# Performance work log

Measured on AMD Instinct MI355X. Metric: run time of the kernel, lower is better.

Reference implementation:

```python
import jax, jax.numpy as jnp
import numpy as np

# config: nsql-350M-like, 8 layers
L, D, H, HD, FF, V, RD, MP = 8, 1024, 16, 64, 4096, 51200, 32, 4


def setup_inputs() -> dict:
    key = jax.random.key(0)
    ks = jax.random.split(key, 8)
    B, S = 1, 1024
    s = 0.02
    return {
        'idx': jax.random.randint(ks[0], (B, S), 0, V),
        'input_pos': jnp.arange(S),
        'emb': jax.random.normal(ks[1], (V, D)) * s,
        'Wqkv': jax.random.normal(ks[2], (L, 3 * D, D)) * s,
        'Wo': jax.random.normal(ks[3], (L, D, D)) * s,
        'ln1_w': jnp.ones((L, D)), 'ln1_b': jnp.zeros((L, D)),
        'fc_in_w': jax.random.normal(ks[4], (L, FF, D)) * s,
        'fc_in_b': jnp.zeros((L, FF)),
        'fc_out_w': jax.random.normal(ks[5], (L, D, FF)) * s,
        'fc_out_b': jnp.zeros((L, D)),
        'lnf_w': jnp.ones((D,)), 'lnf_b': jnp.zeros((D,)),
        'lm_w': jax.random.normal(ks[6], (V, D)) * s,
        'lm_b': jnp.zeros((V,)),
    }


def _layer_norm(x, w, b, eps=1e-5):
    mu = jnp.mean(x, axis=-1, keepdims=True)
    var = jnp.var(x, axis=-1, keepdims=True)
    return (x - mu) * jax.lax.rsqrt(var + eps) * w + b


def _new_gelu(x):
    # transformers NewGELUActivation == tanh-approx gelu
    return jax.nn.gelu(x, approximate=True)


def _sincos(input_pos):
    # create_sinusoidal_positions over rotary_dim, gathered at input_pos
    inv_freq = 1.0 / (10000.0 ** (jnp.arange(0, RD, 2, dtype=jnp.float32) / RD))
    ang = input_pos.astype(jnp.float32)[:, None] * inv_freq          # [S, RD/2]
    # repeat_interleave(..., 2, dim=-1) -> interleaved sin/cos, shape [1,S,1,RD]
    sin = jnp.repeat(jnp.sin(ang), 2, axis=-1)[None, :, None, :]
    cos = jnp.repeat(jnp.cos(ang), 2, axis=-1)[None, :, None, :]
    return sin, cos


def _rotary(x, sin, cos):
    # x: [B,S,H,HD]; GPT-J interleaved rotary on first RD dims
    xr, xp = x[..., :RD], x[..., RD:]
    x1, x2 = xr[..., ::2], xr[..., 1::2]
    rot = jnp.stack((-x2, x1), axis=-1).reshape(xr.shape)  # rotate_every_two
    return jnp.concatenate([xr * cos + rot * sin, xp], axis=-1)


def reference(idx, input_pos, emb, Wqkv, Wo, ln1_w, ln1_b, fc_in_w, fc_in_b,
              fc_out_w, fc_out_b, lnf_w, lnf_b, lm_w, lm_b):
    B, S = idx.shape
    x = emb[idx]                                        # [B,S,D]
    sin, cos = _sincos(input_pos)
    causal = jnp.tril(jnp.ones((S, S), dtype=bool))
    neg = jnp.finfo(x.dtype).min
    ld = D // MP

    def split_heads(t):
        # CodeGen _split_heads with mp_num=4: [B,S,MP,ld] -> [B,S,H,HD]
        return t.reshape(B, S, MP, H // MP, HD).reshape(B, S, H, HD)

    for l in range(L):
        h = _layer_norm(x, ln1_w[l], ln1_b[l])
        qkv = (h @ Wqkv[l].T).reshape(B, S, MP, 3 * ld)
        q, v, k = qkv[..., :ld], qkv[..., ld:2 * ld], qkv[..., 2 * ld:]  # q,v,k order!
        q = _rotary(split_heads(q), sin, cos)
        k = _rotary(split_heads(k), sin, cos)
        vh = split_heads(v)
        q, k, vh = (jnp.transpose(t, (0, 2, 1, 3)) for t in (q, k, vh))  # [B,H,S,HD]
        scores = jnp.einsum('bhqd,bhkd->bhqk', q, k) / jnp.sqrt(jnp.asarray(HD, x.dtype))
        scores = jnp.where(causal, scores, neg)
        att = jax.nn.softmax(scores, axis=-1)
        y = jnp.einsum('bhqk,bhkd->bhqd', att, vh)
        y = jnp.transpose(y, (0, 2, 1, 3)).reshape(B, S, D)
        attn_out = y @ Wo[l].T
        mlp = _new_gelu(h @ fc_in_w[l].T + fc_in_b[l]) @ fc_out_w[l].T + fc_out_b[l]
        x = attn_out + mlp + x                          # parallel block + residual

    x = _layer_norm(x, lnf_w, lnf_b)
    return x @ lm_w.T + lm_b                            # [B,S,V]
```

## Files before the change

### kernel.cpp

```cpp
#include <hip/hip_runtime.h>

#define SQ 1024
#define DIM 1024
#define NH 16
#define HDIM 64
#define FFD 4096
#define NV 51200
#define NL 8
#define LDBUF 5120

typedef __bf16 bf16x8 __attribute__((ext_vector_type(8)));
typedef float f32x4 __attribute__((ext_vector_type(4)));

__device__ __forceinline__ unsigned short f2bf(float f) {
    union { float f; unsigned int i; } v; v.f = f;
    unsigned int r = v.i + 0x7fffu + ((v.i >> 16) & 1u);
    return (unsigned short)(r >> 16);
}
__device__ __forceinline__ float gelu_tanh(float x) {
    float x3 = x * x * x;
    return 0.5f * x * (1.0f + tanhf(0.79788456080286535588f * (x + 0.044715f * x3)));
}

#define GLD16(gp, lp) __builtin_amdgcn_global_load_lds( \
    (__attribute__((address_space(1))) void*)(gp), \
    (__attribute__((address_space(3))) void*)(lp), 16, 0, 0)
#define VMCNT0 asm volatile("s_waitcnt vmcnt(0)" ::: "memory")

__global__ void cvt4_kernel(const float* __restrict__ w0, const float* __restrict__ w1,
                            const float* __restrict__ w2, const float* __restrict__ w3,
                            unsigned short* __restrict__ d0, unsigned short* __restrict__ d1,
                            unsigned short* __restrict__ d2, unsigned short* __restrict__ d3) {
    const int b = blockIdx.x;
    const float* s; unsigned short* d; long off;
    if (b < 1536)      { s = w0; d = d0; off = (long)b * 2048; }
    else if (b < 2048) { s = w1; d = d1; off = (long)(b - 1536) * 2048; }
    else if (b < 4096) { s = w2; d = d2; off = (long)(b - 2048) * 2048; }
    else               { s = w3; d = d3; off = (long)(b - 4096) * 2048; }
    const long i = off + threadIdx.x * 8;
    float4 a = *reinterpret_cast<const float4*>(s + i);
    float4 c = *reinterpret_cast<const float4*>(s + i + 4);
    bf16x8 w;
    w[0] = (__bf16)a.x; w[1] = (__bf16)a.y; w[2] = (__bf16)a.z; w[3] = (__bf16)a.w;
    w[4] = (__bf16)c.x; w[5] = (__bf16)c.y; w[6] = (__bf16)c.z; w[7] = (__bf16)c.w;
    *reinterpret_cast<bf16x8*>(d + i) = w;
}
__global__ void cvt_kernel(const float* __restrict__ src, unsigned short* __restrict__ dst) {
    const long i = ((long)blockIdx.x * 256 + threadIdx.x) * 8;
    float4 a = *reinterpret_cast<const float4*>(src + i);
    float4 b = *reinterpret_cast<const float4*>(src + i + 4);
    bf16x8 w;
    w[0] = (__bf16)a.x; w[1] = (__bf16)a.y; w[2] = (__bf16)a.z; w[3] = (__bf16)a.w;
    w[4] = (__bf16)b.x; w[5] = (__bf16)b.y; w[6] = (__bf16)b.z; w[7] = (__bf16)b.w;
    *reinterpret_cast<bf16x8*>(dst + i) = w;
}

__global__ void sincos_kernel(const int* __restrict__ pos, float2* __restrict__ sc) {
    const int t = blockIdx.x * 256 + threadIdx.x;
    if (t >= SQ * 16) return;
    const int s = t >> 4, i = t & 15;
    const float ang = (float)pos[s] * powf(10000.0f, -(float)i / 16.0f);
    sc[t] = make_float2(sinf(ang), cosf(ang));
}

__global__ void embed_kernel(const int* __restrict__ idx, const float* __restrict__ emb,
                             float* __restrict__ x) {
    const int s = blockIdx.x;
    const int d = threadIdx.x * 4;
    const int row = idx[s];
    *reinterpret_cast<float4*>(x + (long)s * DIM + d) =
        *reinterpret_cast<const float4*>(emb + (long)row * DIM + d);
}

template <bool RED>
__global__ __launch_bounds__(256) void ln_kernel(float* __restrict__ x,
                                                 const float* __restrict__ part,
                                                 const float* __restrict__ w,
                                                 const float* __restrict__ b,
                                                 unsigned short* __restrict__ out) {
    __shared__ float red[8];
    const int s = blockIdx.x, tid = threadIdx.x;
    const long fidx = (long)s * 256 + tid;
    float4 v = reinterpret_cast<const float4*>(x)[fidx];
    if (RED) {
        #pragma unroll
        for (int z = 0; z < 8; z++) {
            float4 p = reinterpret_cast<const float4*>(part + (long)z * SQ * DIM)[fidx];
            v.x += p.x; v.y += p.y; v.z += p.z; v.w += p.w;
        }
        reinterpret_cast<float4*>(x)[fidx] = v;
    }
    float sum = v.x + v.y + v.z + v.w;
    float sq = v.x * v.x + v.y * v.y + v.z * v.z + v.w * v.w;
    #pragma unroll
    for (int off = 32; off; off >>= 1) { sum += __shfl_xor(sum, off); sq += __shfl_xor(sq, off); }
    const int wid = tid >> 6, lane = tid & 63;
    if (lane == 0) { red[wid * 2] = sum; red[wid * 2 + 1] = sq; }
    __syncthreads();
    sum = red[0] + red[2] + red[4] + red[6];
    sq  = red[1] + red[3] + red[5] + red[7];
    const float mu = sum * (1.0f / DIM);
    const float var = sq * (1.0f / DIM) - mu * mu;
    const float rstd = rsqrtf(var + 1e-5f);
    const int d = tid * 4;
    float vv[4] = {v.x, v.y, v.z, v.w};
    ushort4 o;
    unsigned short* op = (unsigned short*)&o;
    #pragma unroll
    for (int j = 0; j < 4; j++)
        op[j] = f2bf((vv[j] - mu) * rstd * w[d + j] + b[d + j]);
    *reinterpret_cast<ushort4*>(out + (long)s * DIM + d) = o;
}

template <int MODE>
__global__ __launch_bounds__(256) void gemm128(const unsigned short* __restrict__ A, int lda,
                                               const unsigned short* __restrict__ B1,
                                               const unsigned short* __restrict__ B2,
                                               const float* __restrict__ bias,
                                               void* __restrict__ C1, void* __restrict__ C2,
                                               const float2* __restrict__ sc,
                                               unsigned short* __restrict__ qt,
                                               unsigned short* __restrict__ kt,
                                               unsigned short* __restrict__ vt) {
    __shared__ __align__(16) unsigned short As[2][128 * 64];
    __shared__ __align__(16) unsigned short Bs[2][128 * 64];
    const int tid = threadIdx.x;
    const int nwg = gridDim.x, qch = nwg >> 3;
    const int sb = (blockIdx.x & 7) * qch + (blockIdx.x >> 3);
    int mb, nb, kz, kt0, ktn;
    if (MODE == 1) { kz = sb & 7; nb = (sb >> 3) & 7; mb = sb >> 6; kt0 = kz * 10; ktn = kt0 + 10; }
    else           { kz = 0; mb = sb & 7; nb = sb >> 3; kt0 = 0; ktn = 16; }
    const int m0 = mb * 128, n0 = nb * 128;
    const int lane = tid & 63, wid = tid >> 6;
    const int l15 = lane & 15, lhi = lane >> 4;
    const int wr = wid >> 1, wc = wid & 1;
    const int sw = l15 & 7;

    const unsigned short* Bbase = B1;
    int nloc = n0;
    if (MODE == 0 && nb >= 24) { Bbase = B2; nloc = n0 - 3072; }

    f32x4 acc[4][4];
    #pragma unroll
    for (int i = 0; i < 4; i++)
        #pragma unroll
        for (int j = 0; j < 4; j++) acc[i][j] = (f32x4){0.f, 0.f, 0.f, 0.f};

    const int wbase = (tid & ~63) * 8;

    auto stage = [&](int buf, int kt_) {
        const int k0 = kt_ << 6;
        #pragma unroll
        for (int i = 0; i < 4; i++) {
            const int e = (i * 256 + tid) * 8;
            const int r = e >> 6;
            const int cs = (((e >> 3) & 7) ^ (r & 7)) * 8;
            GLD16(A + (long)(m0 + r) * lda + k0 + cs, &As[buf][i * 2048 + wbase]);
        }
        if (MODE == 1) {
            const unsigned short* Bp = (k0 < 1024) ? B1 : B2;
            const int ldb = (k0 < 1024) ? 1024 : 4096;
            const int kk = (k0 < 1024) ? k0 : k0 - 1024;
            #pragma unroll
            for (int i = 0; i < 4; i++) {
                const int e = (i * 256 + tid) * 8;
                const int r = e >> 6;
                const int cs = (((e >> 3) & 7) ^ (r & 7)) * 8;
                GLD16(Bp + (long)(n0 + r) * ldb + kk + cs, &Bs[buf][i * 2048 + wbase]);
            }
        } else {
            #pragma unroll
            for (int i = 0; i < 4; i++) {
                const int e = (i * 256 + tid) * 8;
                const int r = e >> 6;
                const int cs = (((e >> 3) & 7) ^ (r & 7)) * 8;
                GLD16(Bbase + (long)(nloc + r) * 1024 + k0 + cs, &Bs[buf][i * 2048 + wbase]);
            }
        }
    };
    auto compute = [&](int buf) {
        #pragma unroll
        for (int ks = 0; ks < 2; ks++) {
            bf16x8 af[4], bfr[4];
            #pragma unroll
            for (int mf = 0; mf < 4; mf++)
                af[mf] = *reinterpret_cast<const bf16x8*>(
                    &As[buf][(wr * 64 + mf * 16 + l15) * 64 + ((ks * 4 + lhi) ^ sw) * 8]);
            #pragma unroll
            for (int nf = 0; nf < 4; nf++)
                bfr[nf] = *reinterpret_cast<const bf16x8*>(
                    &Bs[buf][(wc * 64 + nf * 16 + l15) * 64 + ((ks * 4 + lhi) ^ sw) * 8]);
            #pragma unroll
            for (int mf = 0; mf < 4; mf++)
                #pragma unroll
                for (int nf = 0; nf < 4; nf++)
                    acc[mf][nf] = __builtin_amdgcn_mfma_f32_16x16x32_bf16(af[mf], bfr[nf], acc[mf][nf], 0, 0, 0);
        }
    };

    int cur = 0;
    stage(0, kt0);
    VMCNT0; __syncthreads();
    for (int kt_ = kt0; kt_ < ktn; kt_++) {
        if (kt_ + 1 < ktn) stage(cur ^ 1, kt_ + 1);
        compute(cur);
        if (kt_ + 1 < ktn) { VMCNT0; __syncthreads(); cur ^= 1; }
    }

    if (MODE == 0 && nb < 24) {
        #pragma unroll
        for (int nf = 0; nf < 4; nf++) {
            const int col = n0 + wc * 64 + nf * 16 + l15;
            const int g = col / 768;
            const int r768 = col - g * 768;
            const int sec = r768 >> 8;
            const int off = r768 & 255;
            const int h = g * 4 + (off >> 6);
            const int d = off & 63;
            const bool isrot = (d < 32);
            const int dodd = d & 1;
            #pragma unroll
            for (int mf = 0; mf < 4; mf++) {
                #pragma unroll
                for (int j = 0; j < 4; j++) {
                    const int row = m0 + wr * 64 + mf * 16 + lhi * 4 + j;
                    float v = acc[mf][nf][j];
                    const float pv = __shfl_xor(v, 1);
                    float outv = v;
                    if (isrot && sec != 1) {
                        const float2 scv = sc[row * 16 + (d >> 1)];
                        outv = dodd ? (v * scv.y + pv * scv.x)
                                    : (v * scv.y - pv * scv.x);
                    }
                    if (sec == 0)      qt[((long)(h * SQ + row)) * HDIM + d] = f2bf(outv);
                    else if (sec == 2) kt[((long)(h * SQ + row)) * HDIM + d] = f2bf(outv);
                    else               vt[(long)h * (HDIM * SQ) + (long)d * SQ + row] = f2bf(outv);
                }
            }
        }
    } else {
        #pragma unroll
        for (int nf = 0; nf < 4; nf++) {
            const int col = n0 + wc * 64 + nf * 16 + l15;
            #pragma unroll
            for (int mf = 0; mf < 4; mf++) {
                #pragma unroll
                for (int j = 0; j < 4; j++) {
                    float v = acc[mf][nf][j];
                    const int row = m0 + wr * 64 + mf * 16 + lhi * 4 + j;
                    if (MODE == 0) {
                        v = gelu_tanh(v + bias[col - 3072]);
                        ((unsigned short*)C2)[(long)row * LDBUF + (col - 3072)] = f2bf(v);
                    } else {
                        if (kz == 0) v += bias[col];
                        ((float*)C1)[(long)kz * SQ * DIM + (long)row * DIM + col] = v;
                    }
                }
            }
        }
    }
}

__global__ __launch_bounds__(512) void gemm256(const unsigned short* __restrict__ A,
                                               const unsigned short* __restrict__ B,
                                               const float* __restrict__ bias,
                                               float* __restrict__ C) {
    __shared__ __align__(16) unsigned short As[2][256 * 64];
    __shared__ __align__(16) unsigned short Bs[2][256 * 64];
    const int tid = threadIdx.x;
    const int nwg = gridDim.x, qch = nwg >> 3;
    const int sb = (blockIdx.x & 7) * qch + (blockIdx.x >> 3);
    const int mb = sb & 3, nb = sb >> 2;
    const int m0 = mb * 256, n0 = nb * 256;
    const int lane = tid & 63, wid = tid >> 6;
    const int l15 = lane & 15, lhi = lane >> 4;
    const int wm = wid >> 2, wn = wid & 3;
    const int sw = l15 & 7;

    f32x4 acc[8][4];
    #pragma unroll
    for (int i = 0; i < 8; i++)
        #pragma unroll
        for (int j = 0; j < 4; j++) acc[i][j] = (f32x4){0.f, 0.f, 0.f, 0.f};

    const int wbase = (tid & ~63) * 8;

    auto stage = [&](int buf, int kt) {
        const int k0 = kt << 6;
        #pragma unroll
        for (int i = 0; i < 4; i++) {
            const int e = (i * 512 + tid) * 8;
            const int r = e >> 6;
            const int cs = (((e >> 3) & 7) ^ (r & 7)) * 8;
            GLD16(A + (long)(m0 + r) * 1024 + k0 + cs, &As[buf][i * 4096 + wbase]);
            GLD16(B + (long)(n0 + r) * 1024 + k0 + cs, &Bs[buf][i * 4096 + wbase]);
        }
    };
    auto compute = [&](int buf) {
        #pragma unroll
        for (int ks = 0; ks < 2; ks++) {
            bf16x8 af[8], bfr[4];
            #pragma unroll
            for (int mf = 0; mf < 8; mf++)
                af[mf] = *reinterpret_cast<const bf16x8*>(
                    &As[buf][(wm * 128 + mf * 16 + l15) * 64 + ((ks * 4 + lhi) ^ sw) * 8]);
            #pragma unroll
            for (int nf = 0; nf < 4; nf++)
                bfr[nf] = *reinterpret_cast<const bf16x8*>(
                    &Bs[buf][(wn * 64 + nf * 16 + l15) * 64 + ((ks * 4 + lhi) ^ sw) * 8]);
            #pragma unroll
            for (int mf = 0; mf < 8; mf++)
                #pragma unroll
                for (int nf = 0; nf < 4; nf++)
                    acc[mf][nf] = __builtin_amdgcn_mfma_f32_16x16x32_bf16(af[mf], bfr[nf], acc[mf][nf], 0, 0, 0);
        }
    };

    int cur = 0;
    stage(0, 0);
    VMCNT0; __syncthreads();
    for (int kt = 0; kt < 16; kt++) {
        if (kt < 15) stage(cur ^ 1, kt + 1);
        compute(cur);
        if (kt < 15) { VMCNT0; __syncthreads(); cur ^= 1; }
    }

    #pragma unroll
    for (int nf = 0; nf < 4; nf++) {
        const int col = n0 + wn * 64 + nf * 16 + l15;
        const float bv = bias[col];
        #pragma unroll
        for (int mf = 0; mf < 8; mf++) {
            #pragma unroll
            for (int j = 0; j < 4; j++) {
                const int row = m0 + wm * 128 + mf * 16 + lhi * 4 + j;
                C[(long)row * NV + col] = acc[mf][nf][j] + bv;
            }
        }
    }
}

__global__ __launch_bounds__(256) void attn_kernel(const unsigned short* __restrict__ qt,
                                                   const unsigned short* __restrict__ kt,
                                                   const unsigned short* __restrict__ vt,
                                                   unsigned short* __restrict__ y) {
    __shared__ __align__(16) unsigned short Ks[2][64 * 64];
    __shared__ __align__(16) unsigned short Vs[2][64 * 64];
    __shared__ __align__(16) unsigned short Ps[4][16 * 64];
    const int h = blockIdx.y;
    const int qb = (int)gridDim.x - 1 - (int)blockIdx.x;
    const int tid = threadIdx.x, lane = tid & 63, wid = tid >> 6;
    const int l15 = lane & 15, lhi = lane >> 4;
    const int q0 = qb * 64 + wid * 16;
    const int sw = l15 & 7;

    bf16x8 aq[2];
    {
        const unsigned short* qp = qt + ((long)(h * SQ + q0 + l15)) * HDIM;
        aq[0] = *reinterpret_cast<const bf16x8*>(qp + lhi * 8);
        aq[1] = *reinterpret_cast<const bf16x8*>(qp + 32 + lhi * 8);
    }
    f32x4 o[4];
    #pragma unroll
    for (int nf = 0; nf < 4; nf++) o[nf] = (f32x4){0.f, 0.f, 0.f, 0.f};
    float mrow[4] = {-1e30f, -1e30f, -1e30f, -1e30f};
    float lrow[4] = {0.f, 0.f, 0.f, 0.f};

    const int wb8 = (tid & ~63) * 8;
    auto stageKV = [&](int buf, int kv0) {
        #pragma unroll
        for (int i = 0; i < 2; i++) {
            const int e = (i * 256 + tid) * 8;
            const int r = e >> 6;
            const int cs = (((e >> 3) & 7) ^ (r & 7)) * 8;
            GLD16(kt + ((long)(h * SQ + kv0 + r)) * HDIM + cs, &Ks[buf][i * 2048 + wb8]);
            GLD16(vt + (long)h * (HDIM * SQ) + (long)r * SQ + kv0 + cs, &Vs[buf][i * 2048 + wb8]);
        }
    };

    int cur = 0;
    stageKV(0, 0);
    VMCNT0; __syncthreads();
    for (int kvt = 0; kvt <= qb; kvt++) {
        const int kv0 = kvt * 64;
        if (kvt < qb) stageKV(cur ^ 1, kv0 + 64);

        f32x4 sa[4];
        #pragma unroll
        for (int hc = 0; hc < 4; hc++) sa[hc] = (f32x4){0.f, 0.f, 0.f, 0.f};
        #pragma unroll
        for (int hc = 0; hc < 4; hc++)
            #pragma unroll
            for (int ks = 0; ks < 2; ks++) {
                bf16x8 bk = *reinterpret_cast<const bf16x8*>(
                    &Ks[cur][(hc * 16 + l15) * 64 + ((ks * 4 + lhi) ^ sw) * 8]);
                sa[hc] = __builtin_amdgcn_mfma_f32_16x16x32_bf16(aq[ks], bk, sa[hc], 0, 0, 0);
            }
        float pr[4][4], mb[4];
        #pragma unroll
        for (int j = 0; j < 4; j++) {
            const int qi = q0 + lhi * 4 + j;
            #pragma unroll
            for (int hc = 0; hc < 4; hc++) {
                const int ki = kv0 + hc * 16 + l15;
                const float sv = sa[hc][j] * 0.125f;
                pr[hc][j] = (ki <= qi) ? sv : -1e30f;
            }
            mb[j] = fmaxf(fmaxf(pr[0][j], pr[1][j]), fmaxf(pr[2][j], pr[3][j]));
        }
        #pragma unroll
        for (int off = 1; off < 16; off <<= 1)
            #pragma unroll
            for (int j = 0; j < 4; j++) mb[j] = fmaxf(mb[j], __shfl_xor(mb[j], off));
        float alpha[4], psum[4];
        #pragma unroll
        for (int j = 0; j < 4; j++) {
            const float mn = fmaxf(mrow[j], mb[j]);
            alpha[j] = __expf(mrow[j] - mn);
            mrow[j] = mn;
            psum[j] = 0.f;
            #pragma unroll
            for (int hc = 0; hc < 4; hc++) { pr[hc][j] = __expf(pr[hc][j] - mn); psum[j] += pr[hc][j]; }
        }
        #pragma unroll
        for (int off = 1; off < 16; off <<= 1)
            #pragma unroll
            for (int j = 0; j < 4; j++) psum[j] += __shfl_xor(psum[j], off);
        #pragma unroll
        for (int j = 0; j < 4; j++) lrow[j] = lrow[j] * alpha[j] + psum[j];
        #pragma unroll
        for (int nf = 0; nf < 4; nf++)
            #pragma unroll
            for (int j = 0; j < 4; j++) o[nf][j] *= alpha[j];
        #pragma unroll
        for (int hc = 0; hc < 4; hc++)
            #pragma unroll
            for (int j = 0; j < 4; j++) {
                const int prow = lhi * 4 + j;
                const int pc8 = (hc * 2 + (l15 >> 3)) ^ (prow & 7);
                Ps[wid][prow * 64 + pc8 * 8 + (l15 & 7)] = f2bf(pr[hc][j]);
            }
        bf16x8 ap[2];
        ap[0] = *reinterpret_cast<const bf16x8*>(&Ps[wid][l15 * 64 + ((0 + lhi) ^ sw) * 8]);
        ap[1] = *reinterpret_cast<const bf16x8*>(&Ps[wid][l15 * 64 + ((4 + lhi) ^ sw) * 8]);
        #pragma unroll
        for (int nf = 0; nf < 4; nf++)
            #pragma unroll
            for (int ks2 = 0; ks2 < 2; ks2++) {
                bf16x8 bv = *reinterpret_cast<const bf16x8*>(
                    &Vs[cur][(nf * 16 + l15) * 64 + ((ks2 * 4 + lhi) ^ sw) * 8]);
                o[nf] = __builtin_amdgcn_mfma_f32_16x16x32_bf16(ap[ks2], bv, o[nf], 0, 0, 0);
            }
        if (kvt < qb) { VMCNT0; __syncthreads(); cur ^= 1; }
    }
    #pragma unroll
    for (int nf = 0; nf < 4; nf++)
        #pragma unroll
        for (int j = 0; j < 4; j++) {
            const int row = q0 + lhi * 4 + j;
            y[(long)row * LDBUF + h * HDIM + nf * 16 + l15] = f2bf(o[nf][j] / lrow[j]);
        }
}

extern "C" void kernel_launch(void* const* d_in, const int* in_sizes, int n_in,
                              void* d_out, int out_size, void* d_ws, size_t ws_size,
                              hipStream_t stream) {
    const int* idx    = (const int*)d_in[0];
    const int* pos    = (const int*)d_in[1];
    const float* emb  = (const float*)d_in[2];
    const float* Wqkv = (const float*)d_in[3];
    const float* Wo   = (const float*)d_in[4];
    const float* ln1w = (const float*)d_in[5];
    const float* ln1b = (const float*)d_in[6];
    const float* fciw = (const float*)d_in[7];
    const float* fcib = (const float*)d_in[8];
    const float* fcow = (const float*)d_in[9];
    const float* fcob = (const float*)d_in[10];
    const float* lnfw = (const float*)d_in[11];
    const float* lnfb = (const float*)d_in[12];
    const float* lmw  = (const float*)d_in[13];
    const float* lmb  = (const float*)d_in[14];

    char* ws = (char*)d_ws;
    unsigned short* wbuf = (unsigned short*)ws;   ws += (long)NV * DIM * 2;
    unsigned short* wqkvb = wbuf;
    unsigned short* wob   = wbuf + (long)3072 * 1024;
    unsigned short* fcinb = wob + (long)1024 * 1024;
    unsigned short* fcoutb= fcinb + (long)4096 * 1024;
    float* x           = (float*)ws;          ws += (long)SQ * DIM * 4;
    float* parts       = (float*)ws;          ws += (long)8 * SQ * DIM * 4;
    unsigned short* h  = (unsigned short*)ws; ws += (long)SQ * DIM * 2;
    unsigned short* qt = (unsigned short*)ws; ws += (long)NH * SQ * HDIM * 2;
    unsigned short* kt = (unsigned short*)ws; ws += (long)NH * SQ * HDIM * 2;
    unsigned short* vt = (unsigned short*)ws; ws += (long)NH * SQ * HDIM * 2;
    unsigned short* buf= (unsigned short*)ws; ws += (long)SQ * LDBUF * 2;
    float2* sc         = (float2*)ws;         ws += (long)SQ * 16 * 8;

    sincos_kernel<<<64, 256, 0, stream>>>(pos, sc);
    embed_kernel<<<SQ, 256, 0, stream>>>(idx, emb, x);

    for (int l = 0; l < NL; l++) {
        cvt4_kernel<<<6144, 256, 0, stream>>>(Wqkv + (long)l * 3 * DIM * DIM,
                                              Wo   + (long)l * DIM * DIM,
                                              fciw + (long)l * FFD * DIM,
                                              fcow + (long)l * DIM * FFD,
                                              wqkvb, wob, fcinb, fcoutb);

        if (l == 0) ln_kernel<false><<<SQ, 256, 0, stream>>>(x, nullptr, ln1w, ln1b, h);
        else ln_kernel<true><<<SQ, 256, 0, stream>>>(x, parts, ln1w + (long)l * DIM, ln1b + (long)l * DIM, h);

        gemm128<0><<<448, 256, 0, stream>>>(h, DIM, wqkvb, fcinb, fcib + (long)l * FFD,
                                            nullptr, buf + DIM, sc, qt, kt, vt);
        attn_kernel<<<dim3(16, NH), 256, 0, stream>>>(qt, kt, vt, buf);
        gemm128<1><<<512, 256, 0, stream>>>(buf, LDBUF, wob, fcoutb, fcob + (long)l * DIM,
                                            parts, nullptr, nullptr, nullptr, nullptr, nullptr);
    }
    cvt_kernel<<<25600, 256, 0, stream>>>(lmw, wbuf);
    ln_kernel<true><<<SQ, 256, 0, stream>>>(x, parts, lnfw, lnfb, h);
    gemm256<<<800, 512, 0, stream>>>(h, wbuf, lmb, (float*)d_out);
}
```

Before: 1.197 ms.

## Run attention concurrently with fc_out GEMM and add Wo via read-modify-write

Attention and the fc_out split-K GEMM now run in one launch: the first 256 blocks do causal flash attention while the other 512 compute fc_out partials, which do not depend on attention. The Wo projection then runs as a separate 4-way split-K GEMM that adds its result into the existing partial buffers with read-modify-write. The aim is to fill idle compute units during the unevenly loaded causal attention and to shrink the serial critical path. In exchange, the Wo stage adds an extra fp32 read per element of four partial slices, and the heterogeneous blocks share a larger LDS footprint, which may lower occupancy.

```diff
diff --git a/kernel.cpp b/kernel.cpp
--- a/kernel.cpp
+++ b/kernel.cpp
@@ -112,24 +112,21 @@
     *reinterpret_cast<ushort4*>(out + (long)s * DIM + d) = o;
 }
 
-template <int MODE>
-__global__ __launch_bounds__(256) void gemm128(const unsigned short* __restrict__ A, int lda,
-                                               const unsigned short* __restrict__ B1,
-                                               const unsigned short* __restrict__ B2,
-                                               const float* __restrict__ bias,
-                                               void* __restrict__ C1, void* __restrict__ C2,
-                                               const float2* __restrict__ sc,
-                                               unsigned short* __restrict__ qt,
-                                               unsigned short* __restrict__ kt,
-                                               unsigned short* __restrict__ vt) {
+__global__ __launch_bounds__(256) void gemm_qkv_fcin(const unsigned short* __restrict__ A,
+                                                     const unsigned short* __restrict__ B1,
+                                                     const unsigned short* __restrict__ B2,
+                                                     const float* __restrict__ bias,
+                                                     unsigned short* __restrict__ ffout,
+                                                     const float2* __restrict__ sc,
+                                                     unsigned short* __restrict__ qt,
+                                                     unsigned short* __restrict__ kt,
+                                                     unsigned short* __restrict__ vt) {
     __shared__ __align__(16) unsigned short As[2][128 * 64];
     __shared__ __align__(16) unsigned short Bs[2][128 * 64];
     const int tid = threadIdx.x;
     const int nwg = gridDim.x, qch = nwg >> 3;
     const int sb = (blockIdx.x & 7) * qch + (blockIdx.x >> 3);
-    int mb, nb, kz, kt0, ktn;
-    if (MODE == 1) { kz = sb & 7; nb = (sb >> 3) & 7; mb = sb >> 6; kt0 = kz * 10; ktn = kt0 + 10; }
-    else           { kz = 0; mb = sb & 7; nb = sb >> 3; kt0 = 0; ktn = 16; }
+    const int mb = sb & 7, nb = sb >> 3;
     const int m0 = mb * 128, n0 = nb * 128;
     const int lane = tid & 63, wid = tid >> 6;
     const int l15 = lane & 15, lhi = lane >> 4;
@@ -138,7 +135,7 @@
 
     const unsigned short* Bbase = B1;
     int nloc = n0;
-    if (MODE == 0 && nb >= 24) { Bbase = B2; nloc = n0 - 3072; }
+    if (nb >= 24) { Bbase = B2; nloc = n0 - 3072; }
 
     f32x4 acc[4][4];
     #pragma unroll
@@ -155,27 +152,14 @@
             const int e = (i * 256 + tid) * 8;
             const int r = e >> 6;
             const int cs = (((e >> 3) & 7) ^ (r & 7)) * 8;
-            GLD16(A + (long)(m0 + r) * lda + k0 + cs, &As[buf][i * 2048 + wbase]);
-        }
-        if (MODE == 1) {
-            const unsigned short* Bp = (k0 < 1024) ? B1 : B2;
-            const int ldb = (k0 < 1024) ? 1024 : 4096;
-            const int kk = (k0 < 1024) ? k0 : k0 - 1024;
-            #pragma unroll
-            for (int i = 0; i < 4; i++) {
-                const int e = (i * 256 + tid) * 8;
-                const int r = e >> 6;
-                const int cs = (((e >> 3) & 7) ^ (r & 7)) * 8;
-                GLD16(Bp + (long)(n0 + r) * ldb + kk + cs, &Bs[buf][i * 2048 + wbase]);
-            }
-        } else {
-            #pragma unroll
-            for (int i = 0; i < 4; i++) {
-                const int e = (i * 256 + tid) * 8;
-                const int r = e >> 6;
-                const int cs = (((e >> 3) & 7) ^ (r & 7)) * 8;
-                GLD16(Bbase + (long)(nloc + r) * 1024 + k0 + cs, &Bs[buf][i * 2048 + wbase]);
-            }
+            GLD16(A + (long)(m0 + r) * DIM + k0 + cs, &As[buf][i * 2048 + wbase]);
+        }
+        #pragma unroll
+        for (int i = 0; i < 4; i++) {
+            const int e = (i * 256 + tid) * 8;
+            const int r = e >> 6;
+            const int cs = (((e >> 3) & 7) ^ (r & 7)) * 8;
+            GLD16(Bbase + (long)(nloc + r) * 1024 + k0 + cs, &Bs[buf][i * 2048 + wbase]);
         }
     };
     auto compute = [&](int buf) {
@@ -199,15 +183,15 @@
     };
 
     int cur = 0;
-    stage(0, kt0);
+    stage(0, 0);
     VMCNT0; __syncthreads();
-    for (int kt_ = kt0; kt_ < ktn; kt_++) {
-        if (kt_ + 1 < ktn) stage(cur ^ 1, kt_ + 1);
+    for (int kt_ = 0; kt_ < 16; kt_++) {
+        if (kt_ + 1 < 16) stage(cur ^ 1, kt_ + 1);
         compute(cur);
-        if (kt_ + 1 < ktn) { VMCNT0; __syncthreads(); cur ^= 1; }
-    }
-
-    if (MODE == 0 && nb < 24) {
+        if (kt_ + 1 < 16) { VMCNT0; __syncthreads(); cur ^= 1; }
+    }
+
+    if (nb < 24) {
         #pragma unroll
         for (int nf = 0; nf < 4; nf++) {
             const int col = n0 + wc * 64 + nf * 16 + l15;
@@ -246,16 +230,288 @@
             for (int mf = 0; mf < 4; mf++) {
                 #pragma unroll
                 for (int j = 0; j < 4; j++) {
-                    float v = acc[mf][nf][j];
                     const int row = m0 + wr * 64 + mf * 16 + lhi * 4 + j;
-                    if (MODE == 0) {
-                        v = gelu_tanh(v + bias[col - 3072]);
-                        ((unsigned short*)C2)[(long)row * LDBUF + (col - 3072)] = f2bf(v);
-                    } else {
-                        if (kz == 0) v += bias[col];
-                        ((float*)C1)[(long)kz * SQ * DIM + (long)row * DIM + col] = v;
-                    }
+                    float v = gelu_tanh(acc[mf][nf][j] + bias[col - 3072]);
+                    ffout[(long)row * LDBUF + (col - 3072)] = f2bf(v);
                 }
+            }
+        }
+    }
+}
+
+__global__ __launch_bounds__(256) void attn_fcout(const unsigned short* __restrict__ qt,
+                                                  const unsigned short* __restrict__ kt,
+                                                  const unsigned short* __restrict__ vt,
+                                                  unsigned short* __restrict__ buf,
+                                                  const unsigned short* __restrict__ fcw,
+                                                  const float* __restrict__ fcb,
+                                                  float* __restrict__ parts) {
+    __shared__ __align__(16) unsigned short smem[32768];
+    const int tid = threadIdx.x, lane = tid & 63, wid = tid >> 6;
+    const int l15 = lane & 15, lhi = lane >> 4;
+    const int sw = l15 & 7;
+    const int wbase = (tid & ~63) * 8;
+
+    if (blockIdx.x < 256) {
+        unsigned short* Ks0 = smem;
+        unsigned short* Vs0 = smem + 8192;
+        unsigned short* Psw = smem + 16384 + wid * 1024;
+        const int h = blockIdx.x & 15;
+        const int qb = 15 - ((int)blockIdx.x >> 4);
+        const int q0 = qb * 64 + wid * 16;
+
+        bf16x8 aq[2];
+        {
+            const unsigned short* qp = qt + ((long)(h * SQ + q0 + l15)) * HDIM;
+            aq[0] = *reinterpret_cast<const bf16x8*>(qp + lhi * 8);
+            aq[1] = *reinterpret_cast<const bf16x8*>(qp + 32 + lhi * 8);
+        }
+        f32x4 o[4];
+        #pragma unroll
+        for (int nf = 0; nf < 4; nf++) o[nf] = (f32x4){0.f, 0.f, 0.f, 0.f};
+        float mrow[4] = {-1e30f, -1e30f, -1e30f, -1e30f};
+        float lrow[4] = {0.f, 0.f, 0.f, 0.f};
+
+        auto stageKV = [&](int b, int kv0) {
+            #pragma unroll
+            for (int i = 0; i < 2; i++) {
+                const int e = (i * 256 + tid) * 8;
+                const int r = e >> 6;
+                const int cs = (((e >> 3) & 7) ^ (r & 7)) * 8;
+                GLD16(kt + ((long)(h * SQ + kv0 + r)) * HDIM + cs, Ks0 + b * 4096 + i * 2048 + wbase);
+                GLD16(vt + (long)h * (HDIM * SQ) + (long)r * SQ + kv0 + cs, Vs0 + b * 4096 + i * 2048 + wbase);
+            }
+        };
+
+        int cur = 0;
+        stageKV(0, 0);
+        VMCNT0; __syncthreads();
+        for (int kvt = 0; kvt <= qb; kvt++) {
+            const int kv0 = kvt * 64;
+            if (kvt < qb) stageKV(cur ^ 1, kv0 + 64);
+
+            f32x4 sa[4];
+            #pragma unroll
+            for (int hc = 0; hc < 4; hc++) sa[hc] = (f32x4){0.f, 0.f, 0.f, 0.f};
+            #pragma unroll
+            for (int hc = 0; hc < 4; hc++)
+                #pragma unroll
+                for (int ks = 0; ks < 2; ks++) {
+                    bf16x8 bk = *reinterpret_cast<const bf16x8*>(
+                        Ks0 + cur * 4096 + (hc * 16 + l15) * 64 + ((ks * 4 + lhi) ^ sw) * 8);
+                    sa[hc] = __builtin_amdgcn_mfma_f32_16x16x32_bf16(aq[ks], bk, sa[hc], 0, 0, 0);
+                }
+            float pr[4][4], mb[4];
+            #pragma unroll
+            for (int j = 0; j < 4; j++) {
+                const int qi = q0 + lhi * 4 + j;
+                #pragma unroll
+                for (int hc = 0; hc < 4; hc++) {
+                    const int ki = kv0 + hc * 16 + l15;
+                    const float sv = sa[hc][j] * 0.125f;
+                    pr[hc][j] = (ki <= qi) ? sv : -1e30f;
+                }
+                mb[j] = fmaxf(fmaxf(pr[0][j], pr[1][j]), fmaxf(pr[2][j], pr[3][j]));
+            }
+            #pragma unroll
+            for (int off = 1; off < 16; off <<= 1)
+                #pragma unroll
+                for (int j = 0; j < 4; j++) mb[j] = fmaxf(mb[j], __shfl_xor(mb[j], off));
+            float alpha[4], psum[4];
+            #pragma unroll
+            for (int j = 0; j < 4; j++) {
+                const float mn = fmaxf(mrow[j], mb[j]);
+                alpha[j] = __expf(mrow[j] - mn);
+                mrow[j] = mn;
+                psum[j] = 0.f;
+                #pragma unroll
+                for (int hc = 0; hc < 4; hc++) { pr[hc][j] = __expf(pr[hc][j] - mn); psum[j] += pr[hc][j]; }
+            }
+            #pragma unroll
+            for (int off = 1; off < 16; off <<= 1)
+                #pragma unroll
+                for (int j = 0; j < 4; j++) psum[j] += __shfl_xor(psum[j], off);
+            #pragma unroll
+            for (int j = 0; j < 4; j++) lrow[j] = lrow[j] * alpha[j] + psum[j];
+            #pragma unroll
+            for (int nf = 0; nf < 4; nf++)
+                #pragma unroll
+                for (int j = 0; j < 4; j++) o[nf][j] *= alpha[j];
+            #pragma unroll
+            for (int hc = 0; hc < 4; hc++)
+                #pragma unroll
+                for (int j = 0; j < 4; j++) {
+                    const int prow = lhi * 4 + j;
+                    const int pc8 = (hc * 2 + (l15 >> 3)) ^ (prow & 7);
+                    Psw[prow * 64 + pc8 * 8 + (l15 & 7)] = f2bf(pr[hc][j]);
+                }
+            bf16x8 ap[2];
+            ap[0] = *reinterpret_cast<const bf16x8*>(Psw + l15 * 64 + ((0 + lhi) ^ sw) * 8);
+            ap[1] = *reinterpret_cast<const bf16x8*>(Psw + l15 * 64 + ((4 + lhi) ^ sw) * 8);
+            #pragma unroll
+            for (int nf = 0; nf < 4; nf++)
+                #pragma unroll
+                for (int ks2 = 0; ks2 < 2; ks2++) {
+                    bf16x8 bv = *reinterpret_cast<const bf16x8*>(
+                        Vs0 + cur * 4096 + (nf * 16 + l15) * 64 + ((ks2 * 4 + lhi) ^ sw) * 8);
+                    o[nf] = __builtin_amdgcn_mfma_f32_16x16x32_bf16(ap[ks2], bv, o[nf], 0, 0, 0);
+                }
+            if (kvt < qb) { VMCNT0; __syncthreads(); cur ^= 1; }
+        }
+        #pragma unroll
+        for (int nf = 0; nf < 4; nf++)
+            #pragma unroll
+            for (int j = 0; j < 4; j++) {
+                const int row = q0 + lhi * 4 + j;
+                buf[(long)row * LDBUF + h * HDIM + nf * 16 + l15] = f2bf(o[nf][j] / lrow[j]);
+            }
+    } else {
+        unsigned short* As0 = smem;
+        unsigned short* Bs0 = smem + 16384;
+        const int b2 = (int)blockIdx.x - 256;
+        const int sb = (b2 & 7) * 64 + (b2 >> 3);
+        const int kz = sb & 7, nb = (sb >> 3) & 7, mb = sb >> 6;
+        const int m0 = mb * 128, n0 = nb * 128;
+        const int kt0 = kz * 8;
+        const int wr = wid >> 1, wc = wid & 1;
+        const unsigned short* Aff = buf + DIM;
+
+        f32x4 acc[4][4];
+        #pragma unroll
+        for (int i = 0; i < 4; i++)
+            #pragma unroll
+            for (int j = 0; j < 4; j++) acc[i][j] = (f32x4){0.f, 0.f, 0.f, 0.f};
+
+        auto stage = [&](int bf_, int kt_) {
+            const int k0 = kt_ << 6;
+            #pragma unroll
+            for (int i = 0; i < 4; i++) {
+                const int e = (i * 256 + tid) * 8;
+                const int r = e >> 6;
+                const int cs = (((e >> 3) & 7) ^ (r & 7)) * 8;
+                GLD16(Aff + (long)(m0 + r) * LDBUF + k0 + cs, As0 + bf_ * 8192 + i * 2048 + wbase);
+                GLD16(fcw + (long)(n0 + r) * FFD + k0 + cs, Bs0 + bf_ * 8192 + i * 2048 + wbase);
+            }
+        };
+        auto compute = [&](int bf_) {
+            #pragma unroll
+            for (int ks = 0; ks < 2; ks++) {
+                bf16x8 af[4], bfr[4];
+                #pragma unroll
+                for (int mf = 0; mf < 4; mf++)
+                    af[mf] = *reinterpret_cast<const bf16x8*>(
+                        As0 + bf_ * 8192 + (wr * 64 + mf * 16 + l15) * 64 + ((ks * 4 + lhi) ^ sw) * 8);
+                #pragma unroll
+                for (int nf = 0; nf < 4; nf++)
+                    bfr[nf] = *reinterpret_cast<const bf16x8*>(
+                        Bs0 + bf_ * 8192 + (wc * 64 + nf * 16 + l15) * 64 + ((ks * 4 + lhi) ^ sw) * 8);
+                #pragma unroll
+                for (int mf = 0; mf < 4; mf++)
+                    #pragma unroll
+                    for (int nf = 0; nf < 4; nf++)
+                        acc[mf][nf] = __builtin_amdgcn_mfma_f32_16x16x32_bf16(af[mf], bfr[nf], acc[mf][nf], 0, 0, 0);
+            }
+        };
+
+        int cur = 0;
+        stage(0, kt0);
+        VMCNT0; __syncthreads();
+        for (int t = 0; t < 8; t++) {
+            if (t + 1 < 8) stage(cur ^ 1, kt0 + t + 1);
+            compute(cur);
+            if (t + 1 < 8) { VMCNT0; __syncthreads(); cur ^= 1; }
+        }
+
+        float* P = parts + (long)kz * SQ * DIM;
+        #pragma unroll
+        for (int nf = 0; nf < 4; nf++) {
+            const int col = n0 + wc * 64 + nf * 16 + l15;
+            const float bv = (kz == 0) ? fcb[col] : 0.f;
+            #pragma unroll
+            for (int mf = 0; mf < 4; mf++) {
+                #pragma unroll
+                for (int j = 0; j < 4; j++) {
+                    const int row = m0 + wr * 64 + mf * 16 + lhi * 4 + j;
+                    P[(long)row * DIM + col] = acc[mf][nf][j] + bv;
+                }
+            }
+        }
+    }
+}
+
+__global__ __launch_bounds__(256) void wo_rmw(const unsigned short* __restrict__ buf,
+                                              const unsigned short* __restrict__ wo,
+                                              float* __restrict__ parts) {
+    __shared__ __align__(16) unsigned short As[2][128 * 64];
+    __shared__ __align__(16) unsigned short Bs[2][128 * 64];
+    const int tid = threadIdx.x;
+    const int sb = (blockIdx.x & 7) * 32 + (blockIdx.x >> 3);
+    const int kz = sb & 3, nb = (sb >> 2) & 7, mb = sb >> 5;
+    const int m0 = mb * 128, n0 = nb * 128;
+    const int kt0 = kz * 4;
+    const int lane = tid & 63, wid = tid >> 6;
+    const int l15 = lane & 15, lhi = lane >> 4;
+    const int wr = wid >> 1, wc = wid & 1;
+    const int sw = l15 & 7;
+    const int wbase = (tid & ~63) * 8;
+
+    f32x4 acc[4][4];
+    #pragma unroll
+    for (int i = 0; i < 4; i++)
+        #pragma unroll
+        for (int j = 0; j < 4; j++) acc[i][j] = (f32x4){0.f, 0.f, 0.f, 0.f};
+
+    auto stage = [&](int bf_, int kt_) {
+        const int k0 = kt_ << 6;
+        #pragma unroll
+        for (int i = 0; i < 4; i++) {
+            const int e = (i * 256 + tid) * 8;
+            const int r = e >> 6;
+            const int cs = (((e >> 3) & 7) ^ (r & 7)) * 8;
+            GLD16(buf + (long)(m0 + r) * LDBUF + k0 + cs, &As[bf_][i * 2048 + wbase]);
+            GLD16(wo + (long)(n0 + r) * DIM + k0 + cs, &Bs[bf_][i * 2048 + wbase]);
+        }
+    };
+    auto compute = [&](int bf_) {
+        #pragma unroll
+        for (int ks = 0; ks < 2; ks++) {
+            bf16x8 af[4], bfr[4];
+            #pragma unroll
+            for (int mf = 0; mf < 4; mf++)
+                af[mf] = *reinterpret_cast<const bf16x8*>(
+                    &As[bf_][(wr * 64 + mf * 16 + l15) * 64 + ((ks * 4 + lhi) ^ sw) * 8]);
+            #pragma unroll
+            for (int nf = 0; nf < 4; nf++)
+                bfr[nf] = *reinterpret_cast<const bf16x8*>(
+                    &Bs[bf_][(wc * 64 + nf * 16 + l15) * 64 + ((ks * 4 + lhi) ^ sw) * 8]);
+            #pragma unroll
+            for (int mf = 0; mf < 4; mf++)
+                #pragma unroll
+                for (int nf = 0; nf < 4; nf++)
+                    acc[mf][nf] = __builtin_amdgcn_mfma_f32_16x16x32_bf16(af[mf], bfr[nf], acc[mf][nf], 0, 0, 0);
+        }
+    };
+
+    int cur = 0;
+    stage(0, kt0);
+    VMCNT0; __syncthreads();
+    for (int t = 0; t < 4; t++) {
+        if (t + 1 < 4) stage(cur ^ 1, kt0 + t + 1);
+        compute(cur);
+        if (t + 1 < 4) { VMCNT0; __syncthreads(); cur ^= 1; }
+    }
+
+    float* P = parts + (long)kz * SQ * DIM;
+    #pragma unroll
+    for (int nf = 0; nf < 4; nf++) {
+        const int col = n0 + wc * 64 + nf * 16 + l15;
+        #pragma unroll
+        for (int mf = 0; mf < 4; mf++) {
+            #pragma unroll
+            for (int j = 0; j < 4; j++) {
+                const int row = m0 + wr * 64 + mf * 16 + lhi * 4 + j;
+                const long idx = (long)row * DIM + col;
+                P[idx] += acc[mf][nf][j];
             }
         }
     }
@@ -338,128 +594,6 @@
             }
         }
     }
-}
-
-__global__ __launch_bounds__(256) void attn_kernel(const unsigned short* __restrict__ qt,
-                                                   const unsigned short* __restrict__ kt,
-                                                   const unsigned short* __restrict__ vt,
-                                                   unsigned short* __restrict__ y) {
-    __shared__ __align__(16) unsigned short Ks[2][64 * 64];
-    __shared__ __align__(16) unsigned short Vs[2][64 * 64];
-    __shared__ __align__(16) unsigned short Ps[4][16 * 64];
-    const int h = blockIdx.y;
-    const int qb = (int)gridDim.x - 1 - (int)blockIdx.x;
-    const int tid = threadIdx.x, lane = tid & 63, wid = tid >> 6;
-    const int l15 = lane & 15, lhi = lane >> 4;
-    const int q0 = qb * 64 + wid * 16;
-    const int sw = l15 & 7;
-
-    bf16x8 aq[2];
-    {
-        const unsigned short* qp = qt + ((long)(h * SQ + q0 + l15)) * HDIM;
-        aq[0] = *reinterpret_cast<const bf16x8*>(qp + lhi * 8);
-        aq[1] = *reinterpret_cast<const bf16x8*>(qp + 32 + lhi * 8);
-    }
-    f32x4 o[4];
-    #pragma unroll
-    for (int nf = 0; nf < 4; nf++) o[nf] = (f32x4){0.f, 0.f, 0.f, 0.f};
-    float mrow[4] = {-1e30f, -1e30f, -1e30f, -1e30f};
-    float lrow[4] = {0.f, 0.f, 0.f, 0.f};
-
-    const int wb8 = (tid & ~63) * 8;
-    auto stageKV = [&](int buf, int kv0) {
-        #pragma unroll
-        for (int i = 0; i < 2; i++) {
-            const int e = (i * 256 + tid) * 8;
-            const int r = e >> 6;
-            const int cs = (((e >> 3) & 7) ^ (r & 7)) * 8;
-            GLD16(kt + ((long)(h * SQ + kv0 + r)) * HDIM + cs, &Ks[buf][i * 2048 + wb8]);
-            GLD16(vt + (long)h * (HDIM * SQ) + (long)r * SQ + kv0 + cs, &Vs[buf][i * 2048 + wb8]);
-        }
-    };
-
-    int cur = 0;
-    stageKV(0, 0);
-    VMCNT0; __syncthreads();
-    for (int kvt = 0; kvt <= qb; kvt++) {
-        const int kv0 = kvt * 64;
-        if (kvt < qb) stageKV(cur ^ 1, kv0 + 64);
-
-        f32x4 sa[4];
-        #pragma unroll
-        for (int hc = 0; hc < 4; hc++) sa[hc] = (f32x4){0.f, 0.f, 0.f, 0.f};
-        #pragma unroll
-        for (int hc = 0; hc < 4; hc++)
-            #pragma unroll
-            for (int ks = 0; ks < 2; ks++) {
-                bf16x8 bk = *reinterpret_cast<const bf16x8*>(
-                    &Ks[cur][(hc * 16 + l15) * 64 + ((ks * 4 + lhi) ^ sw) * 8]);
-                sa[hc] = __builtin_amdgcn_mfma_f32_16x16x32_bf16(aq[ks], bk, sa[hc], 0, 0, 0);
-            }
-        float pr[4][4], mb[4];
-        #pragma unroll
-        for (int j = 0; j < 4; j++) {
-            const int qi = q0 + lhi * 4 + j;
-            #pragma unroll
-            for (int hc = 0; hc < 4; hc++) {
-                const int ki = kv0 + hc * 16 + l15;
-                const float sv = sa[hc][j] * 0.125f;
-                pr[hc][j] = (ki <= qi) ? sv : -1e30f;
-            }
-            mb[j] = fmaxf(fmaxf(pr[0][j], pr[1][j]), fmaxf(pr[2][j], pr[3][j]));
-        }
-        #pragma unroll
-        for (int off = 1; off < 16; off <<= 1)
-            #pragma unroll
-            for (int j = 0; j < 4; j++) mb[j] = fmaxf(mb[j], __shfl_xor(mb[j], off));
-        float alpha[4], psum[4];
-        #pragma unroll
-        for (int j = 0; j < 4; j++) {
-            const float mn = fmaxf(mrow[j], mb[j]);
-            alpha[j] = __expf(mrow[j] - mn);
-            mrow[j] = mn;
-            psum[j] = 0.f;
-            #pragma unroll
-            for (int hc = 0; hc < 4; hc++) { pr[hc][j] = __expf(pr[hc][j] - mn); psum[j] += pr[hc][j]; }
-        }
-        #pragma unroll
-        for (int off = 1; off < 16; off <<= 1)
-            #pragma unroll
-            for (int j = 0; j < 4; j++) psum[j] += __shfl_xor(psum[j], off);
-        #pragma unroll
-        for (int j = 0; j < 4; j++) lrow[j] = lrow[j] * alpha[j] + psum[j];
-        #pragma unroll
-        for (int nf = 0; nf < 4; nf++)
-            #pragma unroll
-            for (int j = 0; j < 4; j++) o[nf][j] *= alpha[j];
-        #pragma unroll
-        for (int hc = 0; hc < 4; hc++)
-            #pragma unroll
-            for (int j = 0; j < 4; j++) {
-                const int prow = lhi * 4 + j;
-                const int pc8 = (hc * 2 + (l15 >> 3)) ^ (prow & 7);
-                Ps[wid][prow * 64 + pc8 * 8 + (l15 & 7)] = f2bf(pr[hc][j]);
-            }
-        bf16x8 ap[2];
-        ap[0] = *reinterpret_cast<const bf16x8*>(&Ps[wid][l15 * 64 + ((0 + lhi) ^ sw) * 8]);
-        ap[1] = *reinterpret_cast<const bf16x8*>(&Ps[wid][l15 * 64 + ((4 + lhi) ^ sw) * 8]);
-        #pragma unroll
-        for (int nf = 0; nf < 4; nf++)
-            #pragma unroll
-            for (int ks2 = 0; ks2 < 2; ks2++) {
-                bf16x8 bv = *reinterpret_cast<const bf16x8*>(
-                    &Vs[cur][(nf * 16 + l15) * 64 + ((ks2 * 4 + lhi) ^ sw) * 8]);
-                o[nf] = __builtin_amdgcn_mfma_f32_16x16x32_bf16(ap[ks2], bv, o[nf], 0, 0, 0);
-            }
-        if (kvt < qb) { VMCNT0; __syncthreads(); cur ^= 1; }
-    }
-    #pragma unroll
-    for (int nf = 0; nf < 4; nf++)
-        #pragma unroll
-        for (int j = 0; j < 4; j++) {
-            const int row = q0 + lhi * 4 + j;
-            y[(long)row * LDBUF + h * HDIM + nf * 16 + l15] = f2bf(o[nf][j] / lrow[j]);
-        }
 }
 
 extern "C" void kernel_launch(void* const* d_in, const int* in_sizes, int n_in,
@@ -509,11 +643,10 @@
         if (l == 0) ln_kernel<false><<<SQ, 256, 0, stream>>>(x, nullptr, ln1w, ln1b, h);
         else ln_kernel<true><<<SQ, 256, 0, stream>>>(x, parts, ln1w + (long)l * DIM, ln1b + (long)l * DIM, h);
 
-        gemm128<0><<<448, 256, 0, stream>>>(h, DIM, wqkvb, fcinb, fcib + (long)l * FFD,
-                                            nullptr, buf + DIM, sc, qt, kt, vt);
-        attn_kernel<<<dim3(16, NH), 256, 0, stream>>>(qt, kt, vt, buf);
-        gemm128<1><<<512, 256, 0, stream>>>(buf, LDBUF, wob, fcoutb, fcob + (long)l * DIM,
-                                            parts, nullptr, nullptr, nullptr, nullptr, nullptr);
+        gemm_qkv_fcin<<<448, 256, 0, stream>>>(h, wqkvb, fcinb, fcib + (long)l * FFD,
+                                               buf + DIM, sc, qt, kt, vt);
+        attn_fcout<<<768, 256, 0, stream>>>(qt, kt, vt, buf, fcoutb, fcob + (long)l * DIM, parts);
+        wo_rmw<<<256, 256, 0, stream>>>(buf, wob, parts);
     }
     cvt_kernel<<<25600, 256, 0, stream>>>(lmw, wbuf);
     ln_kernel<true><<<SQ, 256, 0, stream>>>(x, parts, lnfw, lnfb, h);
```

After: 1.094 ms. -8.6%, faster.
